# Kernel tuning notes

Measured on AMD Instinct MI355X. Metric: run time of the kernel, lower is better.

The kernel has to match this reference:

```python
import jax, jax.numpy as jnp
import numpy as np

B, T, C, WD = 8, 2048, 768, 512
TD, CD = 384, 3072   # tokens_dim=0.5*C, channels_dim=4*C
H1 = C               # default hidden of token StyleGLUs
EPS = 1e-6


def _ln(x, g, b):
    mu = jnp.mean(x, -1, keepdims=True)
    v = jnp.mean((x - mu) ** 2, -1, keepdims=True)
    return (x - mu) * jax.lax.rsqrt(v + EPS) * g + b


def _style_glu(x, w, gW, gb, sW, sb, mW, mb):
    # gate linear -> GLU -> style-modulated matmul (modulation folded into einsum)
    h = x @ gW + gb                       # [B,T,H]
    a, gt = jnp.split(h, 2, axis=-1)
    a = a * jax.nn.sigmoid(gt)            # [B,T,H/2]
    s = w @ sW + sb                       # [B,H/2] per-sample style scale
    return jnp.einsum('bth,bh,ho->bto', a, s, mW) + mb


def setup_inputs() -> dict:
    key = jax.random.key(0)
    ks = iter(jax.random.split(key, 40))
    def nrm(*s, sc=0.02):
        return jax.random.normal(next(ks), s, dtype=jnp.float32) * sc
    return dict(
        x=jax.random.normal(next(ks), (B, T, C), dtype=jnp.float32),
        w=jax.random.normal(next(ks), (B, 2, WD), dtype=jnp.float32),
        ln1_g=jnp.ones(C, jnp.float32), ln1_b=jnp.zeros(C, jnp.float32),
        ln2_g=jnp.ones(C, jnp.float32), ln2_b=jnp.zeros(C, jnp.float32),
        g1_W=nrm(C, H1), g1_b=jnp.zeros(H1, jnp.float32),
        s1_W=nrm(WD, H1 // 2), s1_b=jnp.zeros(H1 // 2, jnp.float32),
        m1_W=nrm(H1 // 2, TD, sc=0.05), m1_b=nrm(TD, sc=0.05),
        g2_W=nrm(C, H1), g2_b=jnp.zeros(H1, jnp.float32),
        s2_W=nrm(WD, H1 // 2), s2_b=jnp.zeros(H1 // 2, jnp.float32),
        m2_W=nrm(H1 // 2, TD, sc=0.05), m2_b=nrm(TD, sc=0.05),
        gs_W=nrm(C, CD), gs_b=jnp.zeros(CD, jnp.float32),
        ss_W=nrm(WD, CD // 2), ss_b=jnp.zeros(CD // 2, jnp.float32),
        ms_W=nrm(CD // 2, C, sc=0.05), ms_b=nrm(C, sc=0.05),
        r1_W=nrm(C, C), r1_b=jnp.zeros(C, jnp.float32),
        r2_W=nrm(C // 2, C), r2_b=jnp.zeros(C, jnp.float32),
    )


def reference(x, w, ln1_g, ln1_b, ln2_g, ln2_b,
              g1_W, g1_b, s1_W, s1_b, m1_W, m1_b,
              g2_W, g2_b, s2_W, s2_b, m2_W, m2_b,
              gs_W, gs_b, ss_W, ss_b, ms_W, ms_b,
              r1_W, r1_b, r2_W, r2_b):
    x = _ln(x, ln1_g, ln1_b)
    w0, w1 = w[:, 0], w[:, 1]
    # --- StyleHyperMixer token mixing (eval: dropout/droppath = identity) ---
    h1 = _style_glu(x, w0, g1_W, g1_b, s1_W, s1_b, m1_W, m1_b)  # [B,T,TD]
    h2 = _style_glu(x, w0, g2_W, g2_b, s2_W, s2_b, m2_W, m2_b)  # [B,T,TD]
    mix = jax.nn.gelu(jnp.einsum('btd,btc->bdc', h1, x), approximate=False)  # [B,TD,C]
    x = x + jnp.einsum('btd,bdc->btc', h2, mix)
    # --- style-modulated channel MLP ---
    x = x + _style_glu(_ln(x, ln2_g, ln2_b), w1, gs_W, gs_b, ss_W, ss_b, ms_W, ms_b)
    # --- GLU reduce ---
    h = x @ r1_W + r1_b
    a, gt = jnp.split(h, 2, axis=-1)
    return (a * jax.nn.sigmoid(gt)) @ r2_W + r2_b
```

## Files before the change

### kernel.cpp

```cpp
#include <hip/hip_runtime.h>
#include <hip/hip_bf16.h>
#include <math.h>

#define NB 8
#define NT 2048
#define NC 768
#define ROWS (NB*NT)

typedef __attribute__((ext_vector_type(8))) short s8v;
typedef __attribute__((ext_vector_type(4))) float f4v;

__device__ __forceinline__ unsigned short f2b(float f) {
    unsigned u = __builtin_bit_cast(unsigned, f);
    return (unsigned short)((u + 0x7FFFu + ((u >> 16) & 1u)) >> 16);
}

__device__ __forceinline__ void gll16(const ushort* g, ushort* l) {
    __builtin_amdgcn_global_load_lds(
        (const __attribute__((address_space(1))) void*)g,
        (__attribute__((address_space(3))) void*)l, 16, 0, 0);
}

template<int R>
__device__ __forceinline__ void stageL(ushort* __restrict__ L, const ushort* __restrict__ G,
                                       int ld, int r0, int k0, int lane, int w) {
    int rs = lane >> 2, c = lane & 3;
#pragma unroll
    for (int i = 0; i < R / 64; i++) {
        int ii = w + 4 * i;
        int row = ii * 16 + rs;
        int kc = (c ^ ((row >> 1) & 3)) << 3;
        gll16(G + (long)(r0 + row) * ld + k0 + kc, L + ii * 512);
    }
}

template<int TN, int EPI, bool HASBIAS, bool SPLITK>
__global__ __launch_bounds__(256) void gemm_mfma(
    const ushort* __restrict__ A, const ushort* __restrict__ Bt,
    float* __restrict__ Cf, ushort* __restrict__ Cb,
    int M, int N, int K, int lda, int ldb, int ldc,
    long sA, long sB, long sC, const float* __restrict__ bias)
{
    constexpr int WM = (TN == 128) ? 64 : 32;
    constexpr int TI = WM / 16;
    int zz = blockIdx.z;
    int z  = SPLITK ? (zz >> 2) : zz;
    int kb = SPLITK ? (zz & 3) * (K >> 2) : 0;
    int ke = SPLITK ? kb + (K >> 2) : K;
    const ushort* Az = A + (long)z * sA;
    const ushort* Bz = Bt + (long)z * sB;
    float*  Cfz = Cf ? Cf + (long)z * sC : nullptr;
    ushort* Cbz = Cb ? Cb + (long)z * sC : nullptr;

    int m0 = blockIdx.y * 128, n0 = blockIdx.x * TN;
    __shared__ alignas(16) ushort Al[4096];
    __shared__ alignas(16) ushort Bl[TN * 32];
    int t = threadIdx.x;
    int lane = t & 63, w = t >> 6;
    int wm = (TN == 128) ? (w >> 1) * 64 : w * 32;
    int wn = (TN == 128) ? (w & 1) * 64 : 0;
    int fr = lane & 15, q = lane >> 4;

    f4v acc[TI][4];
#pragma unroll
    for (int i = 0; i < TI; i++)
#pragma unroll
        for (int j = 0; j < 4; j++) acc[i][j] = (f4v)(0.0f);

    for (int k0 = kb; k0 < ke; k0 += 32) {
        stageL<128>(Al, Az, lda, m0, k0, lane, w);
        stageL<TN>(Bl, Bz, ldb, n0, k0, lane, w);
        __syncthreads();
        s8v af[TI], bf[4];
#pragma unroll
        for (int ti = 0; ti < TI; ti++) {
            int r = wm + ti * 16 + fr;
            af[ti] = *(const s8v*)&Al[r * 32 + ((q ^ ((r >> 1) & 3)) << 3)];
        }
#pragma unroll
        for (int tj = 0; tj < 4; tj++) {
            int r = wn + tj * 16 + fr;
            bf[tj] = *(const s8v*)&Bl[r * 32 + ((q ^ ((r >> 1) & 3)) << 3)];
        }
#pragma unroll
        for (int ti = 0; ti < TI; ti++)
#pragma unroll
            for (int tj = 0; tj < 4; tj++)
                acc[ti][tj] = __builtin_amdgcn_mfma_f32_16x16x32_bf16(
                    af[ti], bf[tj], acc[ti][tj], 0, 0, 0);
        __syncthreads();
    }

    int cr0 = q * 4;
#pragma unroll
    for (int ti = 0; ti < TI; ti++) {
#pragma unroll
        for (int tj = 0; tj < 4; tj++) {
            int n = n0 + wn + tj * 16 + fr;
            float bv = HASBIAS ? bias[n] : 0.0f;
#pragma unroll
            for (int r = 0; r < 4; r++) {
                int m = m0 + wm + ti * 16 + cr0 + r;
                long idx = (long)m * ldc + n;
                float v = acc[ti][tj][r] + bv;
                if (EPI == 0) {
                    Cbz[idx] = f2b(v);
                } else if (EPI == 5) {
                    Cfz[idx] = v;
                } else if (EPI == 6) {
                    __hip_atomic_fetch_add(&Cfz[idx], v, __ATOMIC_RELAXED,
                                           __HIP_MEMORY_SCOPE_AGENT);
                } else {
                    v += Cfz[idx];
                    if (EPI == 3) Cfz[idx] = v;
                    if (EPI == 4) Cbz[idx] = f2b(v);
                }
            }
        }
    }
}

template<int TN, bool HAS_S>
__global__ __launch_bounds__(256) void gemm_glu_mfma(
    const ushort* __restrict__ A,
    const ushort* __restrict__ Bt0, const ushort* __restrict__ Bt1,
    ushort* __restrict__ C0, ushort* __restrict__ C1,
    int M, int Nh, int K, int lda,
    const float* __restrict__ bias0, const float* __restrict__ bias1,
    const float* __restrict__ s0, const float* __restrict__ s1, int bofs)
{
    constexpr int WM = (TN == 128) ? 64 : 32;
    constexpr int TI = WM / 16;
    int z = blockIdx.z;
    const ushort* Bt = z ? Bt1 : Bt0;
    ushort* Cb = z ? C1 : C0;
    const float* bias = z ? bias1 : bias0;
    const float* s = z ? s1 : s0;

    int m0 = blockIdx.y * 128, n0 = blockIdx.x * TN;
    __shared__ alignas(16) ushort Al[4096];
    __shared__ alignas(16) ushort B1[TN * 32];
    __shared__ alignas(16) ushort B2[TN * 32];
    int t = threadIdx.x;
    int lane = t & 63, w = t >> 6;
    int wm = (TN == 128) ? (w >> 1) * 64 : w * 32;
    int wn = (TN == 128) ? (w & 1) * 64 : 0;
    int fr = lane & 15, q = lane >> 4;

    f4v acc1[TI][4], acc2[TI][4];
#pragma unroll
    for (int i = 0; i < TI; i++)
#pragma unroll
        for (int j = 0; j < 4; j++) { acc1[i][j] = (f4v)(0.0f); acc2[i][j] = (f4v)(0.0f); }

    for (int k0 = 0; k0 < K; k0 += 32) {
        stageL<TN>(B1, Bt, K, n0, k0, lane, w);
        stageL<TN>(B2, Bt, K, Nh + n0, k0, lane, w);
        stageL<128>(Al, A, lda, m0, k0, lane, w);
        __syncthreads();
        s8v af[TI], b1f[4], b2f[4];
#pragma unroll
        for (int ti = 0; ti < TI; ti++) {
            int r = wm + ti * 16 + fr;
            af[ti] = *(const s8v*)&Al[r * 32 + ((q ^ ((r >> 1) & 3)) << 3)];
        }
#pragma unroll
        for (int tj = 0; tj < 4; tj++) {
            int r = wn + tj * 16 + fr;
            int o = r * 32 + ((q ^ ((r >> 1) & 3)) << 3);
            b1f[tj] = *(const s8v*)&B1[o];
            b2f[tj] = *(const s8v*)&B2[o];
        }
#pragma unroll
        for (int ti = 0; ti < TI; ti++)
#pragma unroll
            for (int tj = 0; tj < 4; tj++) {
                acc1[ti][tj] = __builtin_amdgcn_mfma_f32_16x16x32_bf16(af[ti], b1f[tj], acc1[ti][tj], 0, 0, 0);
                acc2[ti][tj] = __builtin_amdgcn_mfma_f32_16x16x32_bf16(af[ti], b2f[tj], acc2[ti][tj], 0, 0, 0);
            }
        __syncthreads();
    }

    int cr0 = q * 4;
#pragma unroll
    for (int ti = 0; ti < TI; ti++) {
        int bb = ((m0 + wm + ti * 16 + cr0) >> 11) + bofs;
#pragma unroll
        for (int tj = 0; tj < 4; tj++) {
            int n = n0 + wn + tj * 16 + fr;
            float bv = bias[n], bg = bias[Nh + n];
            float sv = HAS_S ? s[(long)bb * Nh + n] : 1.0f;
#pragma unroll
            for (int r = 0; r < 4; r++) {
                int m = m0 + wm + ti * 16 + cr0 + r;
                float vv = acc1[ti][tj][r] + bv;
                float gg = acc2[ti][tj][r] + bg;
                float a = vv * (1.0f / (1.0f + __expf(-gg)));
                if (HAS_S) a *= sv;
                Cb[(long)m * Nh + n] = f2b(a);
            }
        }
    }
}

__global__ __launch_bounds__(256) void gelu_cast_kernel(const float* __restrict__ in,
                                                        ushort* __restrict__ out) {
    int i4 = (blockIdx.x * 256 + threadIdx.x) * 4;
    float4 v = *(const float4*)(in + i4);
    ushort4 o;
    o.x = f2b(0.5f * v.x * (1.0f + erff(v.x * 0.70710678118654752440f)));
    o.y = f2b(0.5f * v.y * (1.0f + erff(v.y * 0.70710678118654752440f)));
    o.z = f2b(0.5f * v.z * (1.0f + erff(v.z * 0.70710678118654752440f)));
    o.w = f2b(0.5f * v.w * (1.0f + erff(v.w * 0.70710678118654752440f)));
    *(ushort4*)(out + i4) = o;
}

template<bool SRC_F32>
__global__ __launch_bounds__(256) void transpose_kernel(const void* __restrict__ src,
                                                        ushort* __restrict__ dst,
                                                        int R, int C, long sS, long sD) {
    int z = blockIdx.z;
    const void* S = SRC_F32 ? (const void*)((const float*)src + (long)z * sS)
                            : (const void*)((const ushort*)src + (long)z * sS);
    ushort* D = dst + (long)z * sD;
    int r0 = blockIdx.y * 64, c0 = blockIdx.x * 64;
    __shared__ ushort T[64][68];
    int t = threadIdx.x;
#pragma unroll
    for (int p = 0; p < 4; p++) {
        int e = p * 256 + t;
        int row = e >> 4, cc = (e & 15) * 4;
        ushort4 v;
        if (SRC_F32) {
            float4 f = *(const float4*)((const float*)S + (long)(r0 + row) * C + c0 + cc);
            v.x = f2b(f.x); v.y = f2b(f.y); v.z = f2b(f.z); v.w = f2b(f.w);
        } else {
            v = *(const ushort4*)((const ushort*)S + (long)(r0 + row) * C + c0 + cc);
        }
        *(ushort4*)&T[row][cc] = v;
    }
    __syncthreads();
#pragma unroll
    for (int p = 0; p < 4; p++) {
        int e = p * 256 + t;
        int crow = e >> 4, rr = (e & 15) * 4;
        ushort4 o;
        o.x = T[rr + 0][crow]; o.y = T[rr + 1][crow];
        o.z = T[rr + 2][crow]; o.w = T[rr + 3][crow];
        *(ushort4*)&D[(long)(c0 + crow) * R + r0 + rr] = o;
    }
}

__global__ __launch_bounds__(256) void prep_kernel(
    const float* __restrict__ g1_W, ushort* __restrict__ g1t,
    const float* __restrict__ g2_W, ushort* __restrict__ g2t,
    const float* __restrict__ m1_W, ushort* __restrict__ m1t,
    const float* __restrict__ m2_W, ushort* __restrict__ m2t,
    const float* __restrict__ gs_W, ushort* __restrict__ gst,
    const float* __restrict__ ms_W, ushort* __restrict__ mst,
    const float* __restrict__ r1_W, ushort* __restrict__ r1t,
    const float* __restrict__ r2_W, ushort* __restrict__ r2t,
    const float* __restrict__ w,
    const float* __restrict__ s1W, const float* __restrict__ s1b,
    const float* __restrict__ s2W, const float* __restrict__ s2b,
    const float* __restrict__ ssW, const float* __restrict__ ssb,
    float* __restrict__ sout)
{
    int b = blockIdx.x, t = threadIdx.x;
    if (b < 23040) {
        const float* W; ushort* Wt; int K, N, lo;
        if      (b < 2304)  { W = g1_W; Wt = g1t; K = 768;  N = 768;  lo = 0; }
        else if (b < 4608)  { W = g2_W; Wt = g2t; K = 768;  N = 768;  lo = 2304; }
        else if (b < 5184)  { W = m1_W; Wt = m1t; K = 384;  N = 384;  lo = 4608; }
        else if (b < 5760)  { W = m2_W; Wt = m2t; K = 384;  N = 384;  lo = 5184; }
        else if (b < 14976) { W = gs_W; Wt = gst; K = 768;  N = 3072; lo = 5760; }
        else if (b < 19584) { W = ms_W; Wt = mst; K = 1536; N = 768;  lo = 14976; }
        else if (b < 21888) { W = r1_W; Wt = r1t; K = 768;  N = 768;  lo = 19584; }
        else                { W = r2_W; Wt = r2t; K = 384;  N = 768;  lo = 21888; }
        int local = b - lo, bx = K >> 6;
        int byi = local / bx, bxi = local - byi * bx;
        int k = bxi * 64 + (t & 63), n = byi * 4 + (t >> 6);
        Wt[(long)n * K + k] = f2b(W[(long)k * N + n]);
    } else {
        int gid = (b - 23040) * 256 + t;
        int bb = gid / 2304;
        int r  = gid % 2304;
        const float* w0 = w + (long)bb * 1024;
        const float* w1 = w0 + 512;
        float acc = 0.f;
        if (r < 384) {
            for (int k = 0; k < 512; k++) acc += w0[k] * s1W[k * 384 + r];
            sout[bb * 384 + r] = acc + s1b[r];
        } else if (r < 768) {
            int c = r - 384;
            for (int k = 0; k < 512; k++) acc += w0[k] * s2W[k * 384 + c];
            sout[3072 + bb * 384 + c] = acc + s2b[c];
        } else {
            int c = r - 768;
            for (int k = 0; k < 512; k++) acc += w1[k] * ssW[k * 1536 + c];
            sout[6144 + bb * 1536 + c] = acc + ssb[c];
        }
    }
}

template<int MODE>
__global__ __launch_bounds__(256) void ln_kernel(const float* __restrict__ x,
                                                 const float* __restrict__ g,
                                                 const float* __restrict__ b,
                                                 float* __restrict__ outf,
                                                 ushort* __restrict__ outb) {
    int row = blockIdx.x;
    const float* xr = x + (long)row * NC;
    int t = threadIdx.x;
    float v0 = xr[t], v1 = xr[t + 256], v2 = xr[t + 512];
    float s = v0 + v1 + v2;
    float s2 = v0 * v0 + v1 * v1 + v2 * v2;
    for (int off = 32; off > 0; off >>= 1) {
        s  += __shfl_down(s, off, 64);
        s2 += __shfl_down(s2, off, 64);
    }
    __shared__ float ls[4], ls2[4];
    int wid = t >> 6, lane = t & 63;
    if (lane == 0) { ls[wid] = s; ls2[wid] = s2; }
    __syncthreads();
    if (t == 0) {
        float ts = ls[0] + ls[1] + ls[2] + ls[3];
        float ts2 = ls2[0] + ls2[1] + ls2[2] + ls2[3];
        float mu = ts * (1.0f / NC);
        float var = ts2 * (1.0f / NC) - mu * mu;
        ls[0] = mu;
        ls2[0] = 1.0f / sqrtf(var + 1e-6f);
    }
    __syncthreads();
    float mu = ls[0], r = ls2[0];
#pragma unroll
    for (int i = 0; i < 3; i++) {
        int c = t + i * 256;
        float vv = (i == 0 ? v0 : (i == 1 ? v1 : v2));
        float o = (vv - mu) * r * g[c] + b[c];
        if (MODE == 2) outf[(long)row * NC + c] = o;
        outb[(long)row * NC + c] = f2b(o);
    }
}

extern "C" void kernel_launch(void* const* d_in, const int* in_sizes, int n_in,
                              void* d_out, int out_size, void* d_ws, size_t ws_size,
                              hipStream_t stream) {
    const float* x     = (const float*)d_in[0];
    const float* w     = (const float*)d_in[1];
    const float* ln1_g = (const float*)d_in[2];
    const float* ln1_b = (const float*)d_in[3];
    const float* ln2_g = (const float*)d_in[4];
    const float* ln2_b = (const float*)d_in[5];
    const float* g1_W  = (const float*)d_in[6];
    const float* g1_b  = (const float*)d_in[7];
    const float* s1_W  = (const float*)d_in[8];
    const float* s1_b  = (const float*)d_in[9];
    const float* m1_W  = (const float*)d_in[10];
    const float* m1_b  = (const float*)d_in[11];
    const float* g2_W  = (const float*)d_in[12];
    const float* g2_b  = (const float*)d_in[13];
    const float* s2_W  = (const float*)d_in[14];
    const float* s2_b  = (const float*)d_in[15];
    const float* m2_W  = (const float*)d_in[16];
    const float* m2_b  = (const float*)d_in[17];
    const float* gs_W  = (const float*)d_in[18];
    const float* gs_b  = (const float*)d_in[19];
    const float* ss_W  = (const float*)d_in[20];
    const float* ss_b  = (const float*)d_in[21];
    const float* ms_W  = (const float*)d_in[22];
    const float* ms_b  = (const float*)d_in[23];
    const float* r1_W  = (const float*)d_in[24];
    const float* r1_b  = (const float*)d_in[25];
    const float* r2_W  = (const float*)d_in[26];
    const float* r2_b  = (const float*)d_in[27];
    float* out = (float*)d_out;
    char* ws = (char*)d_ws;
    char* ob = (char*)d_out;

    float*  XLN = (float*)ws;
    ushort* A1b = (ushort*)(ws + 50331648);
    ushort* g1t = (ushort*)(ws + 62914560);
    ushort* g2t = g1t + 589824;
    ushort* m1t = g2t + 589824;
    ushort* m2t = m1t + 147456;
    ushort* gst = m2t + 147456;
    ushort* mst = gst + 2359296;
    ushort* r1t = mst + 1179648;
    ushort* r2t = r1t + 589824;
    float*  SV  = (float*)(ws + 74711040);
    ushort* H1T = A1b;
    ushort* ASq = A1b;
    ushort* ARq = A1b;

    ushort* XLNb  = (ushort*)(ob + 25165824);
    ushort* XLNT  = (ushort*)(ob + 25165824);
    ushort* A2q   = (ushort*)(ob + 12582912);
    ushort* H2q   = (ushort*)ob;
    ushort* H1q   = (ushort*)(ob + 12582912);
    float*  MIXTf = (float*)(ob + 12582912);
    ushort* MIXTb = (ushort*)(ob + 25165824);
    ushort* X2LNq = (ushort*)(ob + 25165824);
    ushort* X3q   = (ushort*)ob;

    prep_kernel<<<23112, 256, 0, stream>>>(
        g1_W, g1t, g2_W, g2t, m1_W, m1t, m2_W, m2t, gs_W, gst, ms_W, mst,
        r1_W, r1t, r2_W, r2t, w, s1_W, s1_b, s2_W, s2_b, ss_W, ss_b, SV);
    ln_kernel<2><<<ROWS, 256, 0, stream>>>(x, ln1_g, ln1_b, XLN, XLNb);

    gemm_glu_mfma<128, true><<<dim3(3, 128, 2), 256, 0, stream>>>(
        XLNb, g1t, g2t, A1b, A2q, ROWS, 384, 768, 768, g1_b, g2_b, SV, SV + 3072, 0);
    transpose_kernel<true><<<dim3(12, 32, NB), 256, 0, stream>>>(
        XLN, XLNT, 2048, 768, (long)2048 * 768, (long)768 * 2048);
    gemm_mfma<64, 0, true, false><<<dim3(6, 128), 256, 0, stream>>>(
        A2q, m2t, nullptr, H2q, ROWS, 384, 384, 384, 384, 384, 0, 0, 0, m2_b);
    gemm_mfma<64, 0, true, false><<<dim3(6, 128), 256, 0, stream>>>(
        A1b, m1t, nullptr, H1q, ROWS, 384, 384, 384, 384, 384, 0, 0, 0, m1_b);
    transpose_kernel<false><<<dim3(6, 32, NB), 256, 0, stream>>>(
        H1q, H1T, 2048, 384, (long)2048 * 384, (long)384 * 2048);
    hipMemsetAsync(MIXTf, 0, (size_t)NB * 768 * 384 * 4, stream);
    gemm_mfma<128, 6, false, true><<<dim3(3, 6, NB * 4), 256, 0, stream>>>(
        XLNT, H1T, MIXTf, nullptr, 768, 384, 2048, 2048, 2048, 384,
        (long)768 * 2048, (long)384 * 2048, (long)768 * 384, nullptr);
    gelu_cast_kernel<<<2304, 256, 0, stream>>>(MIXTf, MIXTb);
    gemm_mfma<128, 3, false, false><<<dim3(6, 16, NB), 256, 0, stream>>>(
        H2q, MIXTb, XLN, nullptr, 2048, 768, 384, 384, 384, 768,
        (long)2048 * 384, (long)768 * 384, (long)2048 * 768, nullptr);
    ln_kernel<1><<<ROWS, 256, 0, stream>>>(XLN, ln2_g, ln2_b, nullptr, X2LNq);
    for (int ch = 0; ch < 4; ch++) {
        ushort* X2c = X2LNq + (long)ch * 4096 * 768;
        float*  XLNc = XLN + (long)ch * 4096 * 768;
        ushort* X3c = X3q + (long)ch * 4096 * 768;
        gemm_glu_mfma<64, true><<<dim3(24, 32), 256, 0, stream>>>(
            X2c, gst, gst, ASq, ASq, 4096, 1536, 768, 768, gs_b, gs_b,
            SV + 6144, SV + 6144, ch * 2);
        gemm_mfma<64, 4, true, false><<<dim3(12, 32), 256, 0, stream>>>(
            ASq, mst, XLNc, X3c, 4096, 768, 1536, 1536, 1536, 768, 0, 0, 0, ms_b);
    }
    gemm_glu_mfma<64, false><<<dim3(6, 128), 256, 0, stream>>>(
        X3q, r1t, r1t, ARq, ARq, ROWS, 384, 768, 768, r1_b, r1_b, nullptr, nullptr, 0);
    gemm_mfma<128, 5, true, false><<<dim3(6, 128), 256, 0, stream>>>(
        ARq, r2t, out, nullptr, ROWS, 768, 384, 384, 384, 768, 0, 0, 0, r2_b);
}
```

Before: 822.0 us.

## Double-buffer LDS tiles in MFMA GEMM kernels to overlap loads with compute

Both the plain GEMM and the fused GLU GEMM now keep two LDS buffers per operand. The next K-slice is issued with global_load_lds while MFMAs run on the current one, and one barrier per iteration replaces two. This aims to hide global-to-LDS latency behind the matrix math. It doubles LDS use per block, which may lower occupancy. It also relies on the barrier to make the async loads visible, with no explicit wait on the vmcnt counter.

```diff
diff --git a/kernel.cpp b/kernel.cpp
--- a/kernel.cpp
+++ b/kernel.cpp
@@ -43,6 +43,7 @@
 {
     constexpr int WM = (TN == 128) ? 64 : 32;
     constexpr int TI = WM / 16;
+    constexpr int BN = TN * 32;
     int zz = blockIdx.z;
     int z  = SPLITK ? (zz >> 2) : zz;
     int kb = SPLITK ? (zz & 3) * (K >> 2) : 0;
@@ -53,8 +54,8 @@
     ushort* Cbz = Cb ? Cb + (long)z * sC : nullptr;
 
     int m0 = blockIdx.y * 128, n0 = blockIdx.x * TN;
-    __shared__ alignas(16) ushort Al[4096];
-    __shared__ alignas(16) ushort Bl[TN * 32];
+    __shared__ alignas(16) ushort Al[8192];
+    __shared__ alignas(16) ushort Bl[2 * BN];
     int t = threadIdx.x;
     int lane = t & 63, w = t >> 6;
     int wm = (TN == 128) ? (w >> 1) * 64 : w * 32;
@@ -67,20 +68,17 @@
 #pragma unroll
         for (int j = 0; j < 4; j++) acc[i][j] = (f4v)(0.0f);
 
-    for (int k0 = kb; k0 < ke; k0 += 32) {
-        stageL<128>(Al, Az, lda, m0, k0, lane, w);
-        stageL<TN>(Bl, Bz, ldb, n0, k0, lane, w);
-        __syncthreads();
+    auto frag_mfma = [&](const ushort* AB, const ushort* BB) {
         s8v af[TI], bf[4];
 #pragma unroll
         for (int ti = 0; ti < TI; ti++) {
             int r = wm + ti * 16 + fr;
-            af[ti] = *(const s8v*)&Al[r * 32 + ((q ^ ((r >> 1) & 3)) << 3)];
+            af[ti] = *(const s8v*)&AB[r * 32 + ((q ^ ((r >> 1) & 3)) << 3)];
         }
 #pragma unroll
         for (int tj = 0; tj < 4; tj++) {
             int r = wn + tj * 16 + fr;
-            bf[tj] = *(const s8v*)&Bl[r * 32 + ((q ^ ((r >> 1) & 3)) << 3)];
+            bf[tj] = *(const s8v*)&BB[r * 32 + ((q ^ ((r >> 1) & 3)) << 3)];
         }
 #pragma unroll
         for (int ti = 0; ti < TI; ti++)
@@ -88,8 +86,21 @@
             for (int tj = 0; tj < 4; tj++)
                 acc[ti][tj] = __builtin_amdgcn_mfma_f32_16x16x32_bf16(
                     af[ti], bf[tj], acc[ti][tj], 0, 0, 0);
+    };
+
+    int nt = (ke - kb) >> 5;
+    stageL<128>(Al, Az, lda, m0, kb, lane, w);
+    stageL<TN>(Bl, Bz, ldb, n0, kb, lane, w);
+    __syncthreads();
+    int cur = 0;
+    for (int it = 1; it < nt; ++it) {
+        stageL<128>(Al + (cur ^ 1) * 4096, Az, lda, m0, kb + it * 32, lane, w);
+        stageL<TN>(Bl + (cur ^ 1) * BN, Bz, ldb, n0, kb + it * 32, lane, w);
+        frag_mfma(Al + cur * 4096, Bl + cur * BN);
         __syncthreads();
-    }
+        cur ^= 1;
+    }
+    frag_mfma(Al + cur * 4096, Bl + cur * BN);
 
     int cr0 = q * 4;
 #pragma unroll
@@ -131,6 +142,7 @@
 {
     constexpr int WM = (TN == 128) ? 64 : 32;
     constexpr int TI = WM / 16;
+    constexpr int BN = TN * 32;
     int z = blockIdx.z;
     const ushort* Bt = z ? Bt1 : Bt0;
     ushort* Cb = z ? C1 : C0;
@@ -138,9 +150,9 @@
     const float* s = z ? s1 : s0;
 
     int m0 = blockIdx.y * 128, n0 = blockIdx.x * TN;
-    __shared__ alignas(16) ushort Al[4096];
-    __shared__ alignas(16) ushort B1[TN * 32];
-    __shared__ alignas(16) ushort B2[TN * 32];
+    __shared__ alignas(16) ushort Al[8192];
+    __shared__ alignas(16) ushort B1[2 * BN];
+    __shared__ alignas(16) ushort B2[2 * BN];
     int t = threadIdx.x;
     int lane = t & 63, w = t >> 6;
     int wm = (TN == 128) ? (w >> 1) * 64 : w * 32;
@@ -153,23 +165,19 @@
 #pragma unroll
         for (int j = 0; j < 4; j++) { acc1[i][j] = (f4v)(0.0f); acc2[i][j] = (f4v)(0.0f); }
 
-    for (int k0 = 0; k0 < K; k0 += 32) {
-        stageL<TN>(B1, Bt, K, n0, k0, lane, w);
-        stageL<TN>(B2, Bt, K, Nh + n0, k0, lane, w);
-        stageL<128>(Al, A, lda, m0, k0, lane, w);
-        __syncthreads();
+    auto frag_mfma = [&](const ushort* AB, const ushort* BB1, const ushort* BB2) {
         s8v af[TI], b1f[4], b2f[4];
 #pragma unroll
         for (int ti = 0; ti < TI; ti++) {
             int r = wm + ti * 16 + fr;
-            af[ti] = *(const s8v*)&Al[r * 32 + ((q ^ ((r >> 1) & 3)) << 3)];
+            af[ti] = *(const s8v*)&AB[r * 32 + ((q ^ ((r >> 1) & 3)) << 3)];
         }
 #pragma unroll
         for (int tj = 0; tj < 4; tj++) {
             int r = wn + tj * 16 + fr;
             int o = r * 32 + ((q ^ ((r >> 1) & 3)) << 3);
-            b1f[tj] = *(const s8v*)&B1[o];
-            b2f[tj] = *(const s8v*)&B2[o];
+            b1f[tj] = *(const s8v*)&BB1[o];
+            b2f[tj] = *(const s8v*)&BB2[o];
         }
 #pragma unroll
         for (int ti = 0; ti < TI; ti++)
@@ -178,8 +186,24 @@
                 acc1[ti][tj] = __builtin_amdgcn_mfma_f32_16x16x32_bf16(af[ti], b1f[tj], acc1[ti][tj], 0, 0, 0);
                 acc2[ti][tj] = __builtin_amdgcn_mfma_f32_16x16x32_bf16(af[ti], b2f[tj], acc2[ti][tj], 0, 0, 0);
             }
+    };
+
+    int nt = K >> 5;
+    stageL<TN>(B1, Bt, K, n0, 0, lane, w);
+    stageL<TN>(B2, Bt, K, Nh + n0, 0, lane, w);
+    stageL<128>(Al, A, lda, m0, 0, lane, w);
+    __syncthreads();
+    int cur = 0;
+    for (int it = 1; it < nt; ++it) {
+        int k0 = it * 32;
+        stageL<TN>(B1 + (cur ^ 1) * BN, Bt, K, n0, k0, lane, w);
+        stageL<TN>(B2 + (cur ^ 1) * BN, Bt, K, Nh + n0, k0, lane, w);
+        stageL<128>(Al + (cur ^ 1) * 4096, A, lda, m0, k0, lane, w);
+        frag_mfma(Al + cur * 4096, B1 + cur * BN, B2 + cur * BN);
         __syncthreads();
-    }
+        cur ^= 1;
+    }
+    frag_mfma(Al + cur * 4096, B1 + cur * BN, B2 + cur * BN);
 
     int cr0 = q * 4;
 #pragma unroll
```

Result: faster. 794.0 us (median of 2 runs) (-3.4%).
